# Kernel optimization log

Measured on AMD Instinct MI355X. Metric: run time of the kernel, lower is better.

Reference implementation:

```python
import jax, jax.numpy as jnp
import numpy as np

H, KVH, DH = 32, 8, 128        # attention heads, kv heads, head dim (shared by both streams)
G = H // KVH                   # GQA group size
EPS = 1e-6


def rms_norm(x, w):
    xf = x.astype(jnp.float32)
    n = xf * jax.lax.rsqrt(jnp.mean(xf * xf, axis=-1, keepdims=True) + EPS)
    return (n * w).astype(x.dtype)


def apply_rope(x, positions, max_wavelength=10000.0):
    # x: [B, L, h, DH], positions: [B, L]
    d_half = x.shape[-1] // 2
    freq_exponents = (2.0 / x.shape[-1]) * jnp.arange(d_half, dtype=jnp.float32)
    timescale = max_wavelength ** freq_exponents
    radians = positions[..., None].astype(jnp.float32) / timescale          # [B, L, d_half]
    radians = radians[..., None, :]                                         # [B, L, 1, d_half]
    s, c = jnp.sin(radians), jnp.cos(radians)
    xf = x.astype(jnp.float32)
    x1, x2 = xf[..., :d_half], xf[..., d_half:]
    out = jnp.concatenate([x1 * c - x2 * s, x2 * c + x1 * s], axis=-1)
    return out.astype(x.dtype)


def setup_inputs() -> dict:
    key = jax.random.key(0)
    ks = jax.random.split(key, 16)
    B, LV, LE = 2, 1024, 64
    DV, DE = 2560, 1920
    s = 0.02
    inp = {
        "vlm_embeds": jax.random.normal(ks[0], (B, LV, DV), jnp.float32),
        "expert_embeds": jax.random.normal(ks[1], (B, LE, DE), jnp.float32),
        "position_ids": jnp.sort(jax.random.randint(ks[2], (B, LV + LE), 0, 2048), axis=-1),
        "attention_mask": jnp.ones((B, LV + LE, LV + LE), dtype=bool),
        "w_ln_vlm": jnp.ones((DV,), jnp.float32),
        "Wq_vlm": jax.random.normal(ks[3], (DV, H * DH), jnp.float32) * s,
        "Wk_vlm": jax.random.normal(ks[4], (DV, KVH * DH), jnp.float32) * s,
        "Wv_vlm": jax.random.normal(ks[5], (DV, KVH * DH), jnp.float32) * s,
        "Wo_vlm": jax.random.normal(ks[6], (H * DH, DV), jnp.float32) * s,
        "w_ln_exp": jnp.ones((DE,), jnp.float32),
        "Wq_exp": jax.random.normal(ks[7], (DE, H * DH), jnp.float32) * s,
        "Wk_exp": jax.random.normal(ks[8], (DE, KVH * DH), jnp.float32) * s,
        "Wv_exp": jax.random.normal(ks[9], (DE, KVH * DH), jnp.float32) * s,
        "Wo_exp": jax.random.normal(ks[10], (H * DH, DE), jnp.float32) * s,
    }
    return inp


def _mixed_attn_layer(vlm_embeds, expert_embeds,
                      w_ln_vlm, Wq_vlm, Wk_vlm, Wv_vlm, Wo_vlm,
                      w_ln_exp, Wq_exp, Wk_exp, Wv_exp, Wo_exp,
                      position_ids, attention_mask, knowledge_insulation=True):
    B, LV, _ = vlm_embeds.shape
    LE = expert_embeds.shape[1]

    # Stream 0: VLM prefix (knowledge insulation -> no grad into VLM path).
    hv = rms_norm(vlm_embeds, w_ln_vlm)
    qv = (hv @ Wq_vlm).reshape(B, LV, H, DH)
    kv = (hv @ Wk_vlm).reshape(B, LV, KVH, DH)
    vv = (hv @ Wv_vlm).reshape(B, LV, KVH, DH)
    if knowledge_insulation:
        qv = jax.lax.stop_gradient(qv)
        kv = jax.lax.stop_gradient(kv)
        vv = jax.lax.stop_gradient(vv)

    # Stream 1: expert suffix.
    he = rms_norm(expert_embeds, w_ln_exp)
    qe = (he @ Wq_exp).reshape(B, LE, H, DH)
    ke = (he @ Wk_exp).reshape(B, LE, KVH, DH)
    ve = (he @ Wv_exp).reshape(B, LE, KVH, DH)

    # Concatenate streams along the sequence dim, then inline RoPE on q and k.
    q = jnp.concatenate([qv, qe], axis=1)          # [B, L, 32, 128]
    k = jnp.concatenate([kv, ke], axis=1)          # [B, L, 8, 128]
    v = jnp.concatenate([vv, ve], axis=1)
    q = apply_rope(q, position_ids)
    k = apply_rope(k, position_ids)

    # Eager GQA attention in fp32 (matches _eager_attention_forward).
    k_full = jnp.repeat(k, G, axis=2)              # kv-head major, group minor
    v_full = jnp.repeat(v, G, axis=2)
    att = jnp.einsum("bqhd,bkhd->bhqk", q.astype(jnp.float32), k_full.astype(jnp.float32))
    att = att * (DH ** -0.5)
    big_neg = jnp.finfo(jnp.float32).min
    att = jnp.where(attention_mask[:, None, :, :], att, big_neg)
    probs = jax.nn.softmax(att, axis=-1).astype(v_full.dtype)
    out = jnp.einsum("bhqk,bkhd->bqhd", probs, v_full).reshape(B, LV + LE, H * DH)

    # Split back to streams, per-stream output projection + residual.
    out_vlm = vlm_embeds + out[:, :LV] @ Wo_vlm
    out_exp = expert_embeds + out[:, LV:] @ Wo_exp
    return out_vlm, out_exp


def reference(vlm_embeds, expert_embeds, position_ids, attention_mask,
              w_ln_vlm, Wq_vlm, Wk_vlm, Wv_vlm, Wo_vlm,
              w_ln_exp, Wq_exp, Wk_exp, Wv_exp, Wo_exp):
    _, out_exp = _mixed_attn_layer(
        vlm_embeds, expert_embeds,
        w_ln_vlm, Wq_vlm, Wk_vlm, Wv_vlm, Wo_vlm,
        w_ln_exp, Wq_exp, Wk_exp, Wv_exp, Wo_exp,
        position_ids, attention_mask)
    return out_exp
```

## Files before the change

kernel.cpp:

```cpp
#include <hip/hip_runtime.h>
#include <hip/hip_bf16.h>
#include <cstddef>

#define B_  2
#define LV_ 1024
#define LE_ 64
#define S_TOT 1088
#define DV_ 2560
#define DE_ 1920
#define H_  32
#define KVH_ 8
#define DH_ 128
#define HD_ 4096
#define KVD_ 1024
#define NSPL 9

typedef short short8 __attribute__((ext_vector_type(8)));
typedef float f32x4 __attribute__((ext_vector_type(4)));

typedef __hip_bfloat16 bf16;

__device__ inline float b2f(bf16 h) { return __bfloat162float(h); }
__device__ inline bf16 f2b(float f) { return __float2bfloat16(f); }

typedef const __attribute__((address_space(1))) void* gptr_t;
typedef __attribute__((address_space(3))) void* lptr_t;
__device__ inline void gl16(const void* g, void* l) {
  __builtin_amdgcn_global_load_lds((gptr_t)g, (lptr_t)l, 16, 0, 0);
}

#define OFF_HVB   0ul
#define OFF_WKVT  10485760ul
#define OFF_HEB   20971520ul
#define OFF_WQKVT 21463040ul
#define OFF_QE    45056000ul
#define OFF_KBUF  46104576ul
#define OFF_VBUF  50561024ul
#define OFF_AO    59473920ul
#define OFF_OP    0ul
#define OFF_M     18874368ul
#define OFF_L     19021824ul

__global__ __launch_bounds__(256) void rmsnorm_both(
    const float* __restrict__ xv, const float* __restrict__ wv,
    bf16* __restrict__ ov,
    const float* __restrict__ xe, const float* __restrict__ we,
    bf16* __restrict__ oe) {
  int row; const float* x; const float* w; bf16* o; int D;
  if (blockIdx.x < 2048) { row = blockIdx.x;        x = xv; w = wv; o = ov; D = DV_; }
  else                   { row = blockIdx.x - 2048; x = xe; w = we; o = oe; D = DE_; }
  const float4* x4 = (const float4*)(x + (size_t)row * D);
  const float4* w4 = (const float4*)w;
  int D4 = D >> 2;
  float ss = 0.f;
  for (int i = threadIdx.x; i < D4; i += 256) {
    float4 v = x4[i];
    ss += v.x * v.x + v.y * v.y + v.z * v.z + v.w * v.w;
  }
  __shared__ float red[256];
  red[threadIdx.x] = ss; __syncthreads();
  for (int s = 128; s > 0; s >>= 1) {
    if (threadIdx.x < s) red[threadIdx.x] += red[threadIdx.x + s];
    __syncthreads();
  }
  float inv = rsqrtf(red[0] / (float)D + 1e-6f);
  ushort4* o4 = (ushort4*)(o + (size_t)row * D);
  for (int i = threadIdx.x; i < D4; i += 256) {
    float4 v = x4[i], wv2 = w4[i];
    bf16 a = f2b(v.x * inv * wv2.x), b = f2b(v.y * inv * wv2.y);
    bf16 c = f2b(v.z * inv * wv2.z), d = f2b(v.w * inv * wv2.w);
    ushort4 ow;
    ow.x = *(ushort*)&a; ow.y = *(ushort*)&b; ow.z = *(ushort*)&c; ow.w = *(ushort*)&d;
    o4[i] = ow;
  }
}

__device__ inline void tile_tconv(float (*t)[65],
    const float* __restrict__ W, bf16* __restrict__ Wt,
    int K, int N, int n_off, int bx, int by) {
  int n0 = bx * 64, k0 = by * 64;
  int tid = threadIdx.x;
  int c = tid & 63, r4 = tid >> 6;
#pragma unroll 4
  for (int it = 0; it < 16; ++it) {
    int k = it * 4 + r4;
    t[k][c] = W[(size_t)(k0 + k) * N + n0 + c];
  }
  __syncthreads();
#pragma unroll 4
  for (int it = 0; it < 16; ++it) {
    int n = it * 4 + r4;
    Wt[(size_t)(n_off + n0 + n) * K + k0 + c] = f2b(t[c][n]);
  }
}

__global__ __launch_bounds__(256) void tconv_all(
    const float* __restrict__ Wk_vlm, const float* __restrict__ Wv_vlm,
    const float* __restrict__ Wq_exp, const float* __restrict__ Wk_exp,
    const float* __restrict__ Wv_exp,
    bf16* __restrict__ WkvT, bf16* __restrict__ WqkvT) {
  __shared__ float t[64][65];
  int id = blockIdx.x;
  if (id < 640)       tile_tconv(t, Wk_vlm, WkvT, DV_, KVD_, 0,    id % 16, id / 16);
  else if (id < 1280) { id -= 640;  tile_tconv(t, Wv_vlm, WkvT,  DV_, KVD_, 1024, id % 16, id / 16); }
  else if (id < 3200) { id -= 1280; tile_tconv(t, Wq_exp, WqkvT, DE_, HD_,  0,    id % 64, id / 64); }
  else if (id < 3680) { id -= 3200; tile_tconv(t, Wk_exp, WqkvT, DE_, KVD_, 4096, id % 16, id / 16); }
  else                { id -= 3680; tile_tconv(t, Wv_exp, WqkvT, DE_, KVD_, 5120, id % 16, id / 16); }
}

__global__ __launch_bounds__(256) void gemm_fused(
    const bf16* __restrict__ hv, const bf16* __restrict__ WkvT,
    const bf16* __restrict__ he, const bf16* __restrict__ WqkvT,
    bf16* __restrict__ kbuf, bf16* __restrict__ vbuf, bf16* __restrict__ qe) {
  __shared__ ushort As[3][64][32];
  __shared__ ushort Bs[3][64][32];
  int tid = threadIdx.x;
  int lane = tid & 63, w = tid >> 6;
  int lr = lane & 15, quad = lane >> 4;
  int wm = (w >> 1) * 32, wn = (w & 1) * 32;

  bool expert = (blockIdx.x >= 1024);
  const ushort* Ab; const ushort* Bb; int K, nsteps, m0, n0;
  if (!expert) {
    m0 = (int)(blockIdx.x >> 5) * 64; n0 = (int)(blockIdx.x & 31) * 64;
    Ab = (const ushort*)hv; Bb = (const ushort*)WkvT;
    K = DV_; nsteps = DV_ / 32;
  } else {
    int e = (int)blockIdx.x - 1024;
    m0 = (e / 96) * 64; n0 = (e % 96) * 64;
    Ab = (const ushort*)he; Bb = (const ushort*)WqkvT;
    K = DE_; nsteps = DE_ / 32;
  }

  int rr = w * 16 + (lane >> 2);
  int ss = (lane & 3) ^ ((rr >> 1) & 3);
  const ushort* pa = Ab + (size_t)(m0 + rr) * K + ss * 8;
  const ushort* pb = Bb + (size_t)(n0 + rr) * K + ss * 8;

  auto STAGE = [&](int buf, int t) {
    int k0 = t * 32;
    gl16(pa + k0, &As[buf][w * 16][0]);
    gl16(pb + k0, &Bs[buf][w * 16][0]);
  };

  int sslot = (quad ^ ((lr >> 1) & 3)) * 8;

  f32x4 acc[2][2] = {};

  STAGE(0, 0);
  STAGE(1, 1);
  int cur = 0, nxt = 2;
  for (int t = 0; t < nsteps; ++t) {
    int rem = nsteps - t;
    if (rem > 2) {
      STAGE(nxt, t + 2);
      asm volatile("s_waitcnt vmcnt(4)" ::: "memory");
    } else if (rem == 2) {
      asm volatile("s_waitcnt vmcnt(2)" ::: "memory");
    } else {
      asm volatile("s_waitcnt vmcnt(0)" ::: "memory");
    }
    __builtin_amdgcn_s_barrier();

    short8 af[2], bv[2];
#pragma unroll
    for (int i = 0; i < 2; ++i) {
      af[i] = *(const short8*)&As[cur][wm + i * 16 + lr][sslot];
      bv[i] = *(const short8*)&Bs[cur][wn + i * 16 + lr][sslot];
    }
    __builtin_amdgcn_s_setprio(1);
#pragma unroll
    for (int i = 0; i < 2; ++i)
#pragma unroll
      for (int j = 0; j < 2; ++j)
        acc[i][j] = __builtin_amdgcn_mfma_f32_16x16x32_bf16(af[i], bv[j], acc[i][j], 0, 0, 0);
    __builtin_amdgcn_s_setprio(0);

    __builtin_amdgcn_s_barrier();
    cur = (cur == 2) ? 0 : cur + 1;
    nxt = (nxt == 2) ? 0 : nxt + 1;
  }

#pragma unroll
  for (int i = 0; i < 2; ++i) {
    int mm_base = wm + i * 16 + quad * 4;
#pragma unroll
    for (int j = 0; j < 2; ++j) {
      int gn = n0 + wn + j * 16 + lr;
#pragma unroll
      for (int r = 0; r < 4; ++r) {
        int mm = mm_base + r;
        float v = acc[i][j][r];
        if (!expert) {
          int m = m0 + mm;
          int b = m >> 10, s = m & 1023;
          size_t row = (size_t)(b * S_TOT + s);
          if (gn < 1024) kbuf[row * KVD_ + gn] = f2b(v);
          else           vbuf[row * KVD_ + (gn - 1024)] = f2b(v);
        } else {
          int m = m0 + mm;
          int b = m >> 6, l = m & 63;
          if (gn < 4096) {
            qe[(size_t)m * HD_ + gn] = f2b(v);
          } else {
            size_t row = (size_t)(b * S_TOT + LV_ + l);
            if (gn < 5120) kbuf[row * KVD_ + (gn - 4096)] = f2b(v);
            else           vbuf[row * KVD_ + (gn - 5120)] = f2b(v);
          }
        }
      }
    }
  }
}

__global__ __launch_bounds__(256) void gemm_out(
    const bf16* __restrict__ A, const float* __restrict__ W,
    float* __restrict__ out) {
  __shared__ ushort As[128][40];
  __shared__ ushort Bs[64][40];
  int tid = threadIdx.x;
  int lane = tid & 63, wid = tid >> 6;
  int wm = (wid >> 1) * 64, wn = (wid & 1) * 32;
  int n0 = blockIdx.x * 64;
  int k_beg = blockIdx.y * 256;
  int lr = lane & 15, quad = lane >> 4;

  f32x4 acc[4][2] = {};

  int ar = tid >> 2;
  int ac = (tid & 3) * 8;
  const ushort* Aptr = (const ushort*)A + (size_t)ar * HD_ + ac;
  int bn = tid & 63, kg = tid >> 6;
  int bslot_w = ((kg ^ (bn & 3)) * 8);
  int brd = (quad ^ (lr & 3)) * 8;

  for (int k0 = k_beg; k0 < k_beg + 256; k0 += 32) {
    short8 a0 = *(const short8*)(Aptr + k0);
    short8 a1 = *(const short8*)(Aptr + (size_t)64 * HD_ + k0);
    float wv[8];
#pragma unroll
    for (int j = 0; j < 8; ++j)
      wv[j] = W[(size_t)(k0 + kg * 8 + j) * DE_ + n0 + bn];
    short8 bvv;
#pragma unroll
    for (int j = 0; j < 8; ++j) { bf16 h = f2b(wv[j]); bvv[j] = *(short*)&h; }
    __syncthreads();
    *(short8*)&As[ar][ac] = a0;
    *(short8*)&As[64 + ar][ac] = a1;
    *(short8*)&Bs[bn][bslot_w] = bvv;
    __syncthreads();
    short8 af[4], bfr[2];
#pragma unroll
    for (int i = 0; i < 4; ++i)
      af[i]  = *(const short8*)&As[wm + i * 16 + lr][quad * 8];
#pragma unroll
    for (int j = 0; j < 2; ++j)
      bfr[j] = *(const short8*)&Bs[wn + j * 16 + lr][brd];
#pragma unroll
    for (int i = 0; i < 4; ++i)
#pragma unroll
      for (int j = 0; j < 2; ++j)
        acc[i][j] = __builtin_amdgcn_mfma_f32_16x16x32_bf16(af[i], bfr[j], acc[i][j], 0, 0, 0);
  }

#pragma unroll
  for (int i = 0; i < 4; ++i) {
    int m_base = wm + i * 16 + quad * 4;
#pragma unroll
    for (int j = 0; j < 2; ++j) {
      int gn = n0 + wn + j * 16 + lr;
#pragma unroll
      for (int r = 0; r < 4; ++r)
        atomicAdd(&out[(size_t)(m_base + r) * 1920 + gn], acc[i][j][r]);
    }
  }
}

__global__ __launch_bounds__(256) void rope_fused(
    bf16* __restrict__ qe, bf16* __restrict__ kbuf,
    const int* __restrict__ pos_ids) {
  if (blockIdx.x < 128) {
    int row = blockIdx.x;
    int b = row >> 6, l = row & 63;
    float pos = (float)pos_ids[b * S_TOT + LV_ + l];
    bf16* qrow = qe + (size_t)row * HD_;
    for (int p = threadIdx.x; p < H_ * 64; p += 256) {
      int hh = p >> 6, i = p & 63;
      float inv_ts = expf(-9.210340371976184f * (float)i * (1.0f / 64.0f));
      float r = pos * inv_ts;
      float sn = sinf(r), cs = cosf(r);
      float x1 = b2f(qrow[hh * DH_ + i]), x2 = b2f(qrow[hh * DH_ + i + 64]);
      qrow[hh * DH_ + i]      = f2b(x1 * cs - x2 * sn);
      qrow[hh * DH_ + i + 64] = f2b(x2 * cs + x1 * sn);
    }
  } else {
    int bid = blockIdx.x - 128;
    int s = bid % S_TOT, b = bid / S_TOT;
    float pos = (float)pos_ids[b * S_TOT + s];
    size_t base = ((size_t)(b * S_TOT + s)) * KVD_;
    for (int t = threadIdx.x; t < KVH_ * 64; t += 256) {
      int kvh = t >> 6, i = t & 63;
      size_t idx = base + kvh * DH_ + i;
      float inv_ts = expf(-9.210340371976184f * (float)i * (1.0f / 64.0f));
      float r = pos * inv_ts;
      float sn = sinf(r), cs = cosf(r);
      float x1 = b2f(kbuf[idx]), x2 = b2f(kbuf[idx + 64]);
      kbuf[idx]      = f2b(x1 * cs - x2 * sn);
      kbuf[idx + 64] = f2b(x2 * cs + x1 * sn);
    }
  }
}

__global__ __launch_bounds__(256) void attn_part(
    const bf16* __restrict__ qe, const bf16* __restrict__ kbuf,
    const bf16* __restrict__ vbuf,
    float* __restrict__ O_p, float* __restrict__ m_arr,
    float* __restrict__ l_arr) {
  int bh = blockIdx.x & 63;
  int split = blockIdx.x >> 6;
  int h = bh & 31, b = bh >> 5;
  int kvh = h >> 2;
  int tid = threadIdx.x;
  int lane = tid & 63, wid = tid >> 6;
  int lr = lane & 15, quad = lane >> 4;

  __shared__ ushort Ks[64][152];
  __shared__ ushort vTs[128][72];
  __shared__ ushort sc[4][16][72];

  short8 qf[4];
  {
    const ushort* qptr = (const ushort*)qe +
        ((size_t)(b * LE_ + wid * 16 + lr)) * HD_ + h * DH_ + quad * 8;
#pragma unroll
    for (int ks = 0; ks < 4; ++ks) qf[ks] = *(const short8*)(qptr + ks * 32);
  }

  f32x4 Of[8] = {};
  float m_i[4], l_i[4];
#pragma unroll
  for (int r = 0; r < 4; ++r) { m_i[r] = -1e30f; l_i[r] = 0.f; }

  const float scale = 0.08838834764831845f;
  int nch = (split == 8) ? 1 : 2;

  for (int c = 0; c < nch; ++c) {
    int key0 = split * 128 + c * 64;
    __syncthreads();
    {
      int dg = tid & 15, kq = tid >> 4;
#pragma unroll
      for (int it = 0; it < 4; ++it) {
        int key = it * 16 + kq;
        short8 v = *(const short8*)((const ushort*)kbuf +
            ((size_t)(b * S_TOT + key0 + key) * KVH_ + kvh) * DH_ + dg * 8);
        *(short8*)&Ks[key][dg * 8] = v;
      }
    }
    {
      int key = tid & 63, dgrp = tid >> 6;
      const ushort* vp = (const ushort*)vbuf +
          ((size_t)(b * S_TOT + key0 + key) * KVH_ + kvh) * DH_ + dgrp * 32;
      short8 vv[4];
#pragma unroll
      for (int q8 = 0; q8 < 4; ++q8) vv[q8] = *(const short8*)(vp + q8 * 8);
#pragma unroll
      for (int q8 = 0; q8 < 4; ++q8)
#pragma unroll
        for (int j = 0; j < 8; ++j)
          vTs[dgrp * 32 + q8 * 8 + j][key] = (ushort)vv[q8][j];
    }
    __syncthreads();

    f32x4 Sf[4] = {};
#pragma unroll
    for (int kt = 0; kt < 4; ++kt)
#pragma unroll
      for (int ks = 0; ks < 4; ++ks) {
        short8 kf = *(const short8*)&Ks[kt * 16 + lr][quad * 8 + ks * 32];
        Sf[kt] = __builtin_amdgcn_mfma_f32_16x16x32_bf16(qf[ks], kf, Sf[kt], 0, 0, 0);
      }

#pragma unroll
    for (int kt = 0; kt < 4; ++kt) Sf[kt] *= scale;
#pragma unroll
    for (int r = 0; r < 4; ++r) {
      float mx = fmaxf(fmaxf(Sf[0][r], Sf[1][r]), fmaxf(Sf[2][r], Sf[3][r]));
#pragma unroll
      for (int msk = 1; msk < 16; msk <<= 1) mx = fmaxf(mx, __shfl_xor(mx, msk));
      float mn = fmaxf(m_i[r], mx);
      float alpha = __expf(m_i[r] - mn);
      m_i[r] = mn;
      float ls = 0.f;
#pragma unroll
      for (int kt = 0; kt < 4; ++kt) {
        float p = __expf(Sf[kt][r] - mn);
        Sf[kt][r] = p;
        ls += p;
      }
      l_i[r] = l_i[r] * alpha + ls;
#pragma unroll
      for (int nt = 0; nt < 8; ++nt) Of[nt][r] *= alpha;
#pragma unroll
      for (int kt = 0; kt < 4; ++kt) {
        bf16 t = f2b(Sf[kt][r]);
        sc[wid][quad * 4 + r][kt * 16 + lr] = *(ushort*)&t;
      }
    }

#pragma unroll
    for (int ks = 0; ks < 2; ++ks) {
      short8 pf = *(const short8*)&sc[wid][lr][quad * 8 + ks * 32];
#pragma unroll
      for (int nt = 0; nt < 8; ++nt) {
        short8 vf = *(const short8*)&vTs[nt * 16 + lr][quad * 8 + ks * 32];
        Of[nt] = __builtin_amdgcn_mfma_f32_16x16x32_bf16(pf, vf, Of[nt], 0, 0, 0);
      }
    }
  }

  float l_row[4];
#pragma unroll
  for (int r = 0; r < 4; ++r) {
    float l = l_i[r];
#pragma unroll
    for (int msk = 1; msk < 16; msk <<= 1) l += __shfl_xor(l, msk);
    l_row[r] = l;
  }

  size_t rbase = (size_t)split * 4096 + (size_t)bh * 64;
#pragma unroll
  for (int nt = 0; nt < 8; ++nt)
#pragma unroll
    for (int r = 0; r < 4; ++r) {
      int q = wid * 16 + quad * 4 + r;
      O_p[(rbase + q) * 128 + nt * 16 + lr] = Of[nt][r];
    }
  if (lr == 0) {
#pragma unroll
    for (int r = 0; r < 4; ++r) {
      int q = wid * 16 + quad * 4 + r;
      m_arr[rbase + q] = m_i[r];
      l_arr[rbase + q] = l_row[r];
    }
  }
}

__global__ __launch_bounds__(256) void attn_combine(
    const float* __restrict__ O_p, const float* __restrict__ m_arr,
    const float* __restrict__ l_arr, bf16* __restrict__ ao) {
  int t = blockIdx.x * 256 + threadIdx.x;
  int d = t & 127, row = t >> 7;
  float m_g = -1e30f;
#pragma unroll
  for (int s = 0; s < NSPL; ++s) m_g = fmaxf(m_g, m_arr[s * 4096 + row]);
  float denom = 0.f, acc = 0.f;
#pragma unroll
  for (int s = 0; s < NSPL; ++s) {
    float w = __expf(m_arr[s * 4096 + row] - m_g);
    denom += w * l_arr[s * 4096 + row];
    acc   += w * O_p[((size_t)s * 4096 + row) * 128 + d];
  }
  int b = row >> 11, h = (row >> 6) & 31, q = row & 63;
  bf16 o = f2b(acc / denom);
  ((ushort*)ao)[((size_t)(b * 64 + q) * 32 + h) * 128 + d] = *(ushort*)&o;
}

extern "C" void kernel_launch(void* const* d_in, const int* in_sizes, int n_in,
                              void* d_out, int out_size, void* d_ws, size_t ws_size,
                              hipStream_t stream) {
  const float* vlm      = (const float*)d_in[0];
  const float* expe     = (const float*)d_in[1];
  const int*   pos      = (const int*)d_in[2];
  const float* w_ln_vlm = (const float*)d_in[4];
  const float* Wk_vlm   = (const float*)d_in[6];
  const float* Wv_vlm   = (const float*)d_in[7];
  const float* w_ln_exp = (const float*)d_in[9];
  const float* Wq_exp   = (const float*)d_in[10];
  const float* Wk_exp   = (const float*)d_in[11];
  const float* Wv_exp   = (const float*)d_in[12];
  const float* Wo_exp   = (const float*)d_in[13];
  float* out = (float*)d_out;
  char* ws = (char*)d_ws;

  bf16* hv_b  = (bf16*)(ws + OFF_HVB);
  bf16* WkvT  = (bf16*)(ws + OFF_WKVT);
  bf16* he_b  = (bf16*)(ws + OFF_HEB);
  bf16* WqkvT = (bf16*)(ws + OFF_WQKVT);
  bf16* qe    = (bf16*)(ws + OFF_QE);
  bf16* kbuf  = (bf16*)(ws + OFF_KBUF);
  bf16* vbuf  = (bf16*)(ws + OFF_VBUF);
  bf16* ao    = (bf16*)(ws + OFF_AO);
  float* O_p   = (float*)(ws + OFF_OP);
  float* m_arr = (float*)(ws + OFF_M);
  float* l_arr = (float*)(ws + OFF_L);

  hipMemcpyAsync(out, expe, (size_t)B_ * LE_ * DE_ * sizeof(float),
                 hipMemcpyDeviceToDevice, stream);

  rmsnorm_both<<<B_ * LV_ + B_ * LE_, 256, 0, stream>>>(
      vlm, w_ln_vlm, hv_b, expe, w_ln_exp, he_b);

  tconv_all<<<4160, 256, 0, stream>>>(Wk_vlm, Wv_vlm, Wq_exp, Wk_exp, Wv_exp,
                                      WkvT, WqkvT);

  gemm_fused<<<1216, 256, 0, stream>>>(hv_b, WkvT, he_b, WqkvT, kbuf, vbuf, qe);

  rope_fused<<<128 + B_ * S_TOT, 256, 0, stream>>>(qe, kbuf, pos);

  attn_part<<<64 * NSPL, 256, 0, stream>>>(qe, kbuf, vbuf, O_p, m_arr, l_arr);
  attn_combine<<<4096 * 128 / 256, 256, 0, stream>>>(O_p, m_arr, l_arr, ao);

  gemm_out<<<dim3(30, 16), 256, 0, stream>>>(ao, Wo_exp, out);
}
```

Measured before the change: 304.4 us.

## Store V transposed from the QKV GEMM and fold the residual copy into RMSNorm

```diff
diff --git a/kernel.cpp b/kernel.cpp
--- a/kernel.cpp
+++ b/kernel.cpp
@@ -45,12 +45,13 @@
     const float* __restrict__ xv, const float* __restrict__ wv,
     bf16* __restrict__ ov,
     const float* __restrict__ xe, const float* __restrict__ we,
-    bf16* __restrict__ oe) {
-  int row; const float* x; const float* w; bf16* o; int D;
-  if (blockIdx.x < 2048) { row = blockIdx.x;        x = xv; w = wv; o = ov; D = DV_; }
-  else                   { row = blockIdx.x - 2048; x = xe; w = we; o = oe; D = DE_; }
+    bf16* __restrict__ oe, float* __restrict__ outres) {
+  int row; const float* x; const float* w; bf16* o; int D; bool expert;
+  if (blockIdx.x < 2048) { row = blockIdx.x;        x = xv; w = wv; o = ov; D = DV_; expert = false; }
+  else                   { row = blockIdx.x - 2048; x = xe; w = we; o = oe; D = DE_; expert = true; }
   const float4* x4 = (const float4*)(x + (size_t)row * D);
   const float4* w4 = (const float4*)w;
+  float4* res4 = (float4*)(outres + (size_t)row * DE_);
   int D4 = D >> 2;
   float ss = 0.f;
   for (int i = threadIdx.x; i < D4; i += 256) {
@@ -67,6 +68,7 @@
   ushort4* o4 = (ushort4*)(o + (size_t)row * D);
   for (int i = threadIdx.x; i < D4; i += 256) {
     float4 v = x4[i], wv2 = w4[i];
+    if (expert) res4[i] = v;
     bf16 a = f2b(v.x * inv * wv2.x), b = f2b(v.y * inv * wv2.y);
     bf16 c = f2b(v.z * inv * wv2.z), d = f2b(v.w * inv * wv2.w);
     ushort4 ow;
@@ -111,7 +113,7 @@
 __global__ __launch_bounds__(256) void gemm_fused(
     const bf16* __restrict__ hv, const bf16* __restrict__ WkvT,
     const bf16* __restrict__ he, const bf16* __restrict__ WqkvT,
-    bf16* __restrict__ kbuf, bf16* __restrict__ vbuf, bf16* __restrict__ qe) {
+    bf16* __restrict__ kbuf, bf16* __restrict__ vbufT, bf16* __restrict__ qe) {
   __shared__ ushort As[3][64][32];
   __shared__ ushort Bs[3][64][32];
   int tid = threadIdx.x;
@@ -187,26 +189,42 @@
 #pragma unroll
     for (int j = 0; j < 2; ++j) {
       int gn = n0 + wn + j * 16 + lr;
-#pragma unroll
-      for (int r = 0; r < 4; ++r) {
-        int mm = mm_base + r;
-        float v = acc[i][j][r];
-        if (!expert) {
-          int m = m0 + mm;
-          int b = m >> 10, s = m & 1023;
+      int m = m0 + mm_base;
+      if (!expert) {
+        int b = m >> 10, s = m & 1023;
+        if (gn < 1024) {
           size_t row = (size_t)(b * S_TOT + s);
-          if (gn < 1024) kbuf[row * KVD_ + gn] = f2b(v);
-          else           vbuf[row * KVD_ + (gn - 1024)] = f2b(v);
+#pragma unroll
+          for (int r = 0; r < 4; ++r)
+            kbuf[(row + r) * KVD_ + gn] = f2b(acc[i][j][r]);
         } else {
-          int m = m0 + mm;
-          int b = m >> 6, l = m & 63;
-          if (gn < 4096) {
-            qe[(size_t)m * HD_ + gn] = f2b(v);
-          } else {
-            size_t row = (size_t)(b * S_TOT + LV_ + l);
-            if (gn < 5120) kbuf[row * KVD_ + (gn - 4096)] = f2b(v);
-            else           vbuf[row * KVD_ + (gn - 5120)] = f2b(v);
-          }
+          int d = gn - 1024, kvh = d >> 7, dd = d & 127;
+          ushort4 o;
+          bf16 h0 = f2b(acc[i][j][0]), h1 = f2b(acc[i][j][1]);
+          bf16 h2 = f2b(acc[i][j][2]), h3 = f2b(acc[i][j][3]);
+          o.x = *(ushort*)&h0; o.y = *(ushort*)&h1; o.z = *(ushort*)&h2; o.w = *(ushort*)&h3;
+          *(ushort4*)((ushort*)vbufT +
+              ((size_t)(b * KVH_ + kvh) * DH_ + dd) * S_TOT + s) = o;
+        }
+      } else {
+        int b = m >> 6, l = m & 63;
+        if (gn < 4096) {
+#pragma unroll
+          for (int r = 0; r < 4; ++r)
+            qe[(size_t)(m + r) * HD_ + gn] = f2b(acc[i][j][r]);
+        } else if (gn < 5120) {
+          size_t row = (size_t)(b * S_TOT + LV_ + l);
+#pragma unroll
+          for (int r = 0; r < 4; ++r)
+            kbuf[(row + r) * KVD_ + (gn - 4096)] = f2b(acc[i][j][r]);
+        } else {
+          int d = gn - 5120, kvh = d >> 7, dd = d & 127;
+          ushort4 o;
+          bf16 h0 = f2b(acc[i][j][0]), h1 = f2b(acc[i][j][1]);
+          bf16 h2 = f2b(acc[i][j][2]), h3 = f2b(acc[i][j][3]);
+          o.x = *(ushort*)&h0; o.y = *(ushort*)&h1; o.z = *(ushort*)&h2; o.w = *(ushort*)&h3;
+          *(ushort4*)((ushort*)vbufT +
+              ((size_t)(b * KVH_ + kvh) * DH_ + dd) * S_TOT + (LV_ + l)) = o;
         }
       }
     }
@@ -313,7 +331,7 @@
 
 __global__ __launch_bounds__(256) void attn_part(
     const bf16* __restrict__ qe, const bf16* __restrict__ kbuf,
-    const bf16* __restrict__ vbuf,
+    const bf16* __restrict__ vbufT,
     float* __restrict__ O_p, float* __restrict__ m_arr,
     float* __restrict__ l_arr) {
   int bh = blockIdx.x & 63;
@@ -325,8 +343,8 @@
   int lr = lane & 15, quad = lane >> 4;
 
   __shared__ ushort Ks[64][152];
-  __shared__ ushort vTs[128][72];
-  __shared__ ushort sc[4][16][72];
+  __shared__ ushort vTs[128][80];
+  __shared__ ushort sc[4][16][80];
 
   short8 qf[4];
   {
@@ -343,6 +361,8 @@
 
   const float scale = 0.08838834764831845f;
   int nch = (split == 8) ? 1 : 2;
+  const ushort* vtb = (const ushort*)vbufT +
+      (size_t)(b * KVH_ + kvh) * DH_ * S_TOT;
 
   for (int c = 0; c < nch; ++c) {
     int key0 = split * 128 + c * 64;
@@ -358,17 +378,13 @@
       }
     }
     {
-      int key = tid & 63, dgrp = tid >> 6;
-      const ushort* vp = (const ushort*)vbuf +
-          ((size_t)(b * S_TOT + key0 + key) * KVH_ + kvh) * DH_ + dgrp * 32;
-      short8 vv[4];
-#pragma unroll
-      for (int q8 = 0; q8 < 4; ++q8) vv[q8] = *(const short8*)(vp + q8 * 8);
-#pragma unroll
-      for (int q8 = 0; q8 < 4; ++q8)
-#pragma unroll
-        for (int j = 0; j < 8; ++j)
-          vTs[dgrp * 32 + q8 * 8 + j][key] = (ushort)vv[q8][j];
+      int dd = tid >> 3, kk = (tid & 7) * 8;
+#pragma unroll
+      for (int it = 0; it < 4; ++it) {
+        int d = it * 32 + dd;
+        short8 v = *(const short8*)(vtb + (size_t)d * S_TOT + key0 + kk);
+        *(short8*)&vTs[d][kk] = v;
+      }
     }
     __syncthreads();
 
@@ -489,26 +505,23 @@
   bf16* WqkvT = (bf16*)(ws + OFF_WQKVT);
   bf16* qe    = (bf16*)(ws + OFF_QE);
   bf16* kbuf  = (bf16*)(ws + OFF_KBUF);
-  bf16* vbuf  = (bf16*)(ws + OFF_VBUF);
+  bf16* vbufT = (bf16*)(ws + OFF_VBUF);
   bf16* ao    = (bf16*)(ws + OFF_AO);
   float* O_p   = (float*)(ws + OFF_OP);
   float* m_arr = (float*)(ws + OFF_M);
   float* l_arr = (float*)(ws + OFF_L);
 
-  hipMemcpyAsync(out, expe, (size_t)B_ * LE_ * DE_ * sizeof(float),
-                 hipMemcpyDeviceToDevice, stream);
-
   rmsnorm_both<<<B_ * LV_ + B_ * LE_, 256, 0, stream>>>(
-      vlm, w_ln_vlm, hv_b, expe, w_ln_exp, he_b);
+      vlm, w_ln_vlm, hv_b, expe, w_ln_exp, he_b, out);
 
   tconv_all<<<4160, 256, 0, stream>>>(Wk_vlm, Wv_vlm, Wq_exp, Wk_exp, Wv_exp,
                                       WkvT, WqkvT);
 
-  gemm_fused<<<1216, 256, 0, stream>>>(hv_b, WkvT, he_b, WqkvT, kbuf, vbuf, qe);
+  gemm_fused<<<1216, 256, 0, stream>>>(hv_b, WkvT, he_b, WqkvT, kbuf, vbufT, qe);
 
   rope_fused<<<128 + B_ * S_TOT, 256, 0, stream>>>(qe, kbuf, pos);
 
-  attn_part<<<64 * NSPL, 256, 0, stream>>>(qe, kbuf, vbuf, O_p, m_arr, l_arr);
+  attn_part<<<64 * NSPL, 256, 0, stream>>>(qe, kbuf, vbufT, O_p, m_arr, l_arr);
   attn_combine<<<4096 * 128 / 256, 256, 0, stream>>>(O_p, m_arr, l_arr, ao);
 
   gemm_out<<<dim3(30, 16), 256, 0, stream>>>(ao, Wo_exp, out);
```

Result: no change. 303.0 us (-0.5%).
